# Kernel optimization log

Hardware: AMD Instinct MI355X
Metric: run time of the kernel (lower is better)

Reference implementation:

```python
import jax, jax.numpy as jnp
import numpy as np

# Tree / model dimensions
L = 1024          # number of leaves (batch rows of x)
F = 128           # num_features
H = 128           # num_dense_units
C = 10            # output_dim (num classes)
N = 2 * L - 1     # full binary tree node count
SPLICE = [0, F*H, F*H+H, F*H+H+H*H, F*H+2*H+H*H, F*H+2*H+H*H+H*C, F*H+2*H+H*H+H*C+C]
D = SPLICE[-1]    # 34314 = flattened sub-MLP weight count (layer_shape)
MIN_DIST = 1e-7


def setup_inputs() -> dict:
    key = jax.random.key(0)
    k1, k2, k3 = jax.random.split(key, 3)
    x = jax.random.normal(k1, (L, F), dtype=jnp.float32)
    # per-node AdditionLayer weight vectors (trainable deltas)
    W = jax.random.normal(k2, (N, D), dtype=jnp.float32) * 0.02
    heights = jax.random.uniform(k3, (N,), dtype=jnp.float32)
    p = (np.arange(N) - 1) // 2
    p[0] = 0  # root self-parent; root is excluded from the mut-distance term
    parent = jnp.asarray(p, dtype=jnp.int32)
    leaf_idx = jnp.arange(L - 1, N, dtype=jnp.int32)  # leaves in traversal order
    return {"x": x, "W": W, "heights": heights, "parent": parent, "leaf_idx": leaf_idx}


def reference(x, W, heights, parent, leaf_idx):
    n = W.shape[0]
    depth = int(np.log2(n + 1))
    # Effective weights per node = sum of AdditionLayer deltas along root->node path.
    # Level-by-level parent gather (parents at level d-1 are already accumulated).
    eff = W
    for d in range(1, depth):
        s, e = 2 ** d - 1, 2 ** (d + 1) - 1
        eff = eff.at[s:e].add(eff[parent[s:e]])

    # delta_tensor: root uses squared diff vs zero input (= sum(W_root^2));
    # every other node: curr - input = W_node, so sum|W_node| / mut_distance.
    mut = jnp.maximum(jnp.abs(heights - heights[parent]), MIN_DIST)  # [n]
    l1 = jnp.sum(jnp.abs(W), axis=1)                                 # [n]
    delta = jnp.sum(W[0] ** 2) + jnp.sum(l1[1:] / mut[1:])
    delta = jnp.reshape(delta, (1,))

    # Leaf sub-MLP: splice each leaf's effective weight vector into kernels/biases
    wl = eff[leaf_idx]                                  # [L, D]
    Lf = wl.shape[0]
    W0 = wl[:, SPLICE[0]:SPLICE[1]].reshape(Lf, F, H)
    b0 = wl[:, SPLICE[1]:SPLICE[2]]
    W1 = wl[:, SPLICE[2]:SPLICE[3]].reshape(Lf, H, H)
    b1 = wl[:, SPLICE[3]:SPLICE[4]]
    W2 = wl[:, SPLICE[4]:SPLICE[5]].reshape(Lf, H, C)
    b2 = wl[:, SPLICE[5]:SPLICE[6]]
    h = jax.nn.relu(jnp.einsum('lf,lfh->lh', x, W0) + b0)
    h = jax.nn.relu(jnp.einsum('lh,lhk->lk', h, W1) + b1)
    out = jax.nn.softmax(jnp.einsum('lh,lhc->lc', h, W2) + b2, axis=-1)
    return (out, delta)
```

## Files before the change

kernel.cpp:

```cpp
#include <hip/hip_runtime.h>

#define LN 1024
#define FF 128
#define HH 128
#define CC 10
#define DD 34314
#define OFF_W0 0
#define OFF_B0 16384
#define OFF_W1 16512
#define OFF_B1 32896
#define OFF_W2 33024
#define OFF_B2 34304

__global__ void init_delta(float* delta) { *delta = 0.f; }

__device__ __forceinline__ float invmut(const float* h, int node, int par) {
    return 1.f / fmaxf(fabsf(h[node] - h[par]), 1e-7f);
}

__global__ __launch_bounds__(1024, 4) void fused_kernel(const float* __restrict__ W,
                                                        const float* __restrict__ x,
                                                        const float* __restrict__ heights,
                                                        float* __restrict__ out,
                                                        float* __restrict__ delta_out) {
    const int bid  = blockIdx.x;
    const int m    = ((bid & 7) << 5) | (bid >> 3);
    const int tid  = threadIdx.x;
    const int lane = tid & 63;
    const int wv   = tid >> 6;
    const int j2   = lane;

    int path[9];
    {
        int n = 255 + m;
#pragma unroll
        for (int k = 0; k < 9; ++k) { path[k] = n; n = (n - 1) >> 1; }
    }
    const float* R[15];
#pragma unroll
    for (int k = 0; k < 9; ++k) R[k] = W + (size_t)path[k] * DD;
    const int n9a = 511 + 2 * m, n9b = n9a + 1;
    R[9]  = W + (size_t)n9a * DD;
    R[10] = W + (size_t)n9b * DD;
#pragma unroll
    for (int q = 0; q < 4; ++q) R[11 + q] = W + (size_t)(1023 + 4 * m + q) * DD;

    float wgt[15];
#pragma unroll
    for (int k = 0; k < 8; ++k)
        wgt[k] = ((m & ((1 << k) - 1)) == 0) ? invmut(heights, path[k], path[k + 1]) : 0.f;
    wgt[8]  = 0.f;
    wgt[9]  = invmut(heights, n9a, path[0]);
    wgt[10] = invmut(heights, n9b, path[0]);
#pragma unroll
    for (int q = 0; q < 4; ++q)
        wgt[11 + q] = invmut(heights, 1023 + 4 * m + q, (q < 2) ? n9a : n9b);
    const float sqmask = (m == 0) ? 1.f : 0.f;

    __shared__ float ins[4][HH];
    __shared__ float part[4][16][HH];
    __shared__ float lgts[4][CC];
    __shared__ float red[16];

    if (tid < 512) { const int q = tid >> 7, t = tid & 127; ins[q][t] = x[(4 * m + q) * FF + t]; }
    if (tid < 4 * CC) ((float*)lgts)[tid] = 0.f;

    float dacc = 0.f, sacc = 0.f;
    __syncthreads();

#pragma unroll
    for (int layer = 0; layer < 2; ++layer) {
        const int offW = layer ? OFF_W1 : OFF_W0;
        const int offB = layer ? OFF_B1 : OFF_B0;
        const float2* S2[15];
#pragma unroll
        for (int r = 0; r < 15; ++r) S2[r] = reinterpret_cast<const float2*>(R[r] + offW);

        float yx[4], yy[4];
#pragma unroll
        for (int q = 0; q < 4; ++q) { yx[q] = 0.f; yy[q] = 0.f; }

#pragma unroll 2
        for (int i = 0; i < 8; ++i) {
            const int f   = (wv << 3) + i;
            const int off = (f << 6) + j2;
            float ex = 0.f, ey = 0.f;
#pragma unroll
            for (int k = 0; k < 9; ++k) {
                const float2 w = S2[k][off];
                ex += w.x; ey += w.y;
                dacc += (fabsf(w.x) + fabsf(w.y)) * wgt[k];
                if (k == 8) sacc += w.x * w.x + w.y * w.y;
            }
            const float2 wa0 = S2[9][off];
            const float2 wa1 = S2[10][off];
            dacc += (fabsf(wa0.x) + fabsf(wa0.y)) * wgt[9];
            dacc += (fabsf(wa1.x) + fabsf(wa1.y)) * wgt[10];
#pragma unroll
            for (int q = 0; q < 4; ++q) {
                const float2 wb = S2[11 + q][off];
                dacc += (fabsf(wb.x) + fabsf(wb.y)) * wgt[11 + q];
                const float2 wa = (q < 2) ? wa0 : wa1;
                const float xv = ins[q][f];
                yx[q] += xv * (ex + wa.x + wb.x);
                yy[q] += xv * (ey + wa.y + wb.y);
            }
        }
#pragma unroll
        for (int q = 0; q < 4; ++q)
            *reinterpret_cast<float2*>(&part[q][wv][2 * j2]) = make_float2(yx[q], yy[q]);
        __syncthreads();

        if (tid < 512) {
            const int q = tid >> 7, col = tid & 127;
            float eb = 0.f;
#pragma unroll
            for (int k = 0; k < 9; ++k) {
                const float v = R[k][offB + col];
                eb += v;
                if (q == 0) { dacc += fabsf(v) * wgt[k]; if (k == 8) sacc += v * v; }
            }
            const float a0 = R[9][offB + col];
            const float a1 = R[10][offB + col];
            if (q == 0) dacc += fabsf(a0) * wgt[9];
            if (q == 2) dacc += fabsf(a1) * wgt[10];
            const float bq = R[11 + q][offB + col];
            dacc += fabsf(bq) * wgt[11 + q];
            float s = eb + ((q < 2) ? a0 : a1) + bq;
#pragma unroll
            for (int w = 0; w < 16; ++w) s += part[q][w][col];
            ins[q][col] = fmaxf(s, 0.f);
        }
        __syncthreads();
    }

    {
        const float2* S2[15];
#pragma unroll
        for (int r = 0; r < 15; ++r) S2[r] = reinterpret_cast<const float2*>(R[r] + OFF_W2);
        if (tid < 640) {
            const int h  = tid / 5;
            const int c0 = (tid - 5 * h) * 2;
            float ex = 0.f, ey = 0.f;
#pragma unroll
            for (int k = 0; k < 9; ++k) {
                const float2 w = S2[k][tid];
                ex += w.x; ey += w.y;
                dacc += (fabsf(w.x) + fabsf(w.y)) * wgt[k];
                if (k == 8) sacc += w.x * w.x + w.y * w.y;
            }
            const float2 wa0 = S2[9][tid];
            const float2 wa1 = S2[10][tid];
            dacc += (fabsf(wa0.x) + fabsf(wa0.y)) * wgt[9];
            dacc += (fabsf(wa1.x) + fabsf(wa1.y)) * wgt[10];
#pragma unroll
            for (int q = 0; q < 4; ++q) {
                const float2 wb = S2[11 + q][tid];
                dacc += (fabsf(wb.x) + fabsf(wb.y)) * wgt[11 + q];
                const float2 wa = (q < 2) ? wa0 : wa1;
                const float hv = ins[q][h];
                atomicAdd(&lgts[q][c0],     hv * (ex + wa.x + wb.x));
                atomicAdd(&lgts[q][c0 + 1], hv * (ey + wa.y + wb.y));
            }
        }
        __syncthreads();
        if (tid < CC) {
            float eb = 0.f;
#pragma unroll
            for (int k = 0; k < 9; ++k) {
                const float v = R[k][OFF_B2 + tid];
                eb += v;
                dacc += fabsf(v) * wgt[k];
                if (k == 8) sacc += v * v;
            }
            const float a0 = R[9][OFF_B2 + tid];
            const float a1 = R[10][OFF_B2 + tid];
            dacc += fabsf(a0) * wgt[9] + fabsf(a1) * wgt[10];
#pragma unroll
            for (int q = 0; q < 4; ++q) {
                const float bq = R[11 + q][OFF_B2 + tid];
                dacc += fabsf(bq) * wgt[11 + q];
                lgts[q][tid] += eb + ((q < 2) ? a0 : a1) + bq;
            }
        }
        __syncthreads();
    }

    if (tid < 4) {
        const int q = tid;
        float mx = lgts[q][0];
#pragma unroll
        for (int c = 1; c < CC; ++c) mx = fmaxf(mx, lgts[q][c]);
        float e[CC], s = 0.f;
#pragma unroll
        for (int c = 0; c < CC; ++c) { e[c] = expf(lgts[q][c] - mx); s += e[c]; }
        const float inv = 1.f / s;
#pragma unroll
        for (int c = 0; c < CC; ++c) out[(4 * m + q) * CC + c] = e[c] * inv;
    }

    float v = dacc + sacc * sqmask;
    for (int o = 32; o > 0; o >>= 1) v += __shfl_down(v, o);
    if (lane == 0) red[wv] = v;
    __syncthreads();
    if (tid == 0) {
        float s = 0.f;
#pragma unroll
        for (int w = 0; w < 16; ++w) s += red[w];
        atomicAdd(delta_out, s);
    }
}

extern "C" void kernel_launch(void* const* d_in, const int* in_sizes, int n_in,
                              void* d_out, int out_size, void* d_ws, size_t ws_size,
                              hipStream_t stream) {
    const float* x       = (const float*)d_in[0];
    const float* W       = (const float*)d_in[1];
    const float* heights = (const float*)d_in[2];

    float* out   = (float*)d_out;
    float* delta = (float*)d_out + LN * CC;

    init_delta<<<1, 1, 0, stream>>>(delta);
    fused_kernel<<<256, 1024, 0, stream>>>(W, x, heights, out, delta);
}
```

Baseline: 97.08 us.

## Split fused MLP kernel into three per-layer kernels with more blocks

Splits the single 256-block fused kernel into three kernels, one per layer. The two large layers use 1024 blocks of 512 threads, each handling a quarter of the input rows, and write partial products to workspace; the next kernel sums them and applies bias and ReLU. This is meant to raise parallelism and occupancy across the GPU's compute units for the bandwidth-bound weight reads. The cost is extra launches, workspace round-trips, and redundant setup and bias reads per block.

```diff
diff --git a/kernel.cpp b/kernel.cpp
--- a/kernel.cpp
+++ b/kernel.cpp
@@ -18,25 +18,11 @@
     return 1.f / fmaxf(fabsf(h[node] - h[par]), 1e-7f);
 }
 
-__global__ __launch_bounds__(1024, 4) void fused_kernel(const float* __restrict__ W,
-                                                        const float* __restrict__ x,
-                                                        const float* __restrict__ heights,
-                                                        float* __restrict__ out,
-                                                        float* __restrict__ delta_out) {
-    const int bid  = blockIdx.x;
-    const int m    = ((bid & 7) << 5) | (bid >> 3);
-    const int tid  = threadIdx.x;
-    const int lane = tid & 63;
-    const int wv   = tid >> 6;
-    const int j2   = lane;
-
-    int path[9];
-    {
-        int n = 255 + m;
-#pragma unroll
-        for (int k = 0; k < 9; ++k) { path[k] = n; n = (n - 1) >> 1; }
-    }
-    const float* R[15];
+__device__ __forceinline__ void setup(const float* W, const float* heights, int m,
+                                      int* path, const float** R, float* wgt) {
+    int n = 255 + m;
+#pragma unroll
+    for (int k = 0; k < 9; ++k) { path[k] = n; n = (n - 1) >> 1; }
 #pragma unroll
     for (int k = 0; k < 9; ++k) R[k] = W + (size_t)path[k] * DD;
     const int n9a = 511 + 2 * m, n9b = n9a + 1;
@@ -44,8 +30,6 @@
     R[10] = W + (size_t)n9b * DD;
 #pragma unroll
     for (int q = 0; q < 4; ++q) R[11 + q] = W + (size_t)(1023 + 4 * m + q) * DD;
-
-    float wgt[15];
 #pragma unroll
     for (int k = 0; k < 8; ++k)
         wgt[k] = ((m & ((1 << k) - 1)) == 0) ? invmut(heights, path[k], path[k + 1]) : 0.f;
@@ -55,110 +39,247 @@
 #pragma unroll
     for (int q = 0; q < 4; ++q)
         wgt[11 + q] = invmut(heights, 1023 + 4 * m + q, (q < 2) ? n9a : n9b);
-    const float sqmask = (m == 0) ? 1.f : 0.f;
-
-    __shared__ float ins[4][HH];
-    __shared__ float part[4][16][HH];
+}
+
+__global__ __launch_bounds__(512, 8) void k1_w0(const float* __restrict__ W,
+                                                const float* __restrict__ x,
+                                                const float* __restrict__ heights,
+                                                float* __restrict__ ws_y0,
+                                                float* __restrict__ delta_out) {
+    const int bid = blockIdx.x;
+    const int m   = (bid & 7) * 32 + ((bid >> 3) >> 2);
+    const int qt  = (bid >> 3) & 3;
+    const int tid = threadIdx.x, lane = tid & 63, wv = tid >> 6, j2 = lane;
+
+    int path[9]; const float* R[15]; float wgt[15];
+    setup(W, heights, m, path, R, wgt);
+    const float sq = (m == 0) ? 1.f : 0.f;
+
+    __shared__ float xs[4][32];
+    __shared__ float part[4][8][HH];
+    __shared__ float red[8];
+
+    if (tid < 128) { const int q = tid >> 5, f = tid & 31; xs[q][f] = x[(4 * m + q) * FF + qt * 32 + f]; }
+    float dacc = 0.f, sacc = 0.f;
+    float yx[4] = {0.f, 0.f, 0.f, 0.f}, yy[4] = {0.f, 0.f, 0.f, 0.f};
+    __syncthreads();
+
+    const float2* S2[15];
+#pragma unroll
+    for (int r = 0; r < 15; ++r) S2[r] = reinterpret_cast<const float2*>(R[r] + OFF_W0);
+
+#pragma unroll
+    for (int i = 0; i < 4; ++i) {
+        const int fl  = (wv << 2) + i;
+        const int off = (((qt << 5) + fl) << 6) + j2;
+        float ex = 0.f, ey = 0.f;
+#pragma unroll
+        for (int k = 0; k < 9; ++k) {
+            const float2 w = S2[k][off];
+            ex += w.x; ey += w.y;
+            dacc += (fabsf(w.x) + fabsf(w.y)) * wgt[k];
+            if (k == 8) sacc += w.x * w.x + w.y * w.y;
+        }
+        const float2 wa0 = S2[9][off];
+        const float2 wa1 = S2[10][off];
+        dacc += (fabsf(wa0.x) + fabsf(wa0.y)) * wgt[9];
+        dacc += (fabsf(wa1.x) + fabsf(wa1.y)) * wgt[10];
+#pragma unroll
+        for (int q = 0; q < 4; ++q) {
+            const float2 wb = S2[11 + q][off];
+            dacc += (fabsf(wb.x) + fabsf(wb.y)) * wgt[11 + q];
+            const float2 wa = (q < 2) ? wa0 : wa1;
+            const float xv = xs[q][fl];
+            yx[q] += xv * (ex + wa.x + wb.x);
+            yy[q] += xv * (ey + wa.y + wb.y);
+        }
+    }
+#pragma unroll
+    for (int q = 0; q < 4; ++q)
+        *reinterpret_cast<float2*>(&part[q][wv][2 * j2]) = make_float2(yx[q], yy[q]);
+    __syncthreads();
+    {
+        const int q = tid >> 7, col = tid & 127;
+        float s = 0.f;
+#pragma unroll
+        for (int w = 0; w < 8; ++w) s += part[q][w][col];
+        ws_y0[(((m << 2) + qt) << 9) + tid] = s;
+    }
+    float v = dacc + sacc * sq;
+    for (int o = 32; o > 0; o >>= 1) v += __shfl_down(v, o);
+    if (lane == 0) red[wv] = v;
+    __syncthreads();
+    if (tid == 0) {
+        float s = 0.f;
+#pragma unroll
+        for (int w = 0; w < 8; ++w) s += red[w];
+        atomicAdd(delta_out, s);
+    }
+}
+
+__global__ __launch_bounds__(512, 8) void k2_w1(const float* __restrict__ W,
+                                                const float* __restrict__ heights,
+                                                const float* __restrict__ ws_y0,
+                                                float* __restrict__ ws_y1,
+                                                float* __restrict__ delta_out) {
+    const int bid = blockIdx.x;
+    const int m   = (bid & 7) * 32 + ((bid >> 3) >> 2);
+    const int qt  = (bid >> 3) & 3;
+    const int tid = threadIdx.x, lane = tid & 63, wv = tid >> 6, j2 = lane;
+
+    int path[9]; const float* R[15]; float wgt[15];
+    setup(W, heights, m, path, R, wgt);
+    const float sq = (m == 0) ? 1.f : 0.f;
+
+    __shared__ float hs[4][HH];
+    __shared__ float part[4][8][HH];
+    __shared__ float red[8];
+    float dacc = 0.f, sacc = 0.f;
+
+    {
+        const int q = tid >> 7, col = tid & 127;
+        float s = 0.f;
+#pragma unroll
+        for (int qq = 0; qq < 4; ++qq) s += ws_y0[(((m << 2) + qq) << 9) + tid];
+        float eb = 0.f;
+#pragma unroll
+        for (int k = 0; k < 9; ++k) {
+            const float v = R[k][OFF_B0 + col];
+            eb += v;
+            if (qt == 0 && q == 0) { dacc += fabsf(v) * wgt[k]; if (k == 8) sacc += v * v; }
+        }
+        const float a0 = R[9][OFF_B0 + col];
+        const float a1 = R[10][OFF_B0 + col];
+        if (qt == 0 && q == 0) dacc += fabsf(a0) * wgt[9];
+        if (qt == 0 && q == 2) dacc += fabsf(a1) * wgt[10];
+        const float bq = R[11 + q][OFF_B0 + col];
+        if (qt == 0) dacc += fabsf(bq) * wgt[11 + q];
+        hs[q][col] = fmaxf(s + eb + ((q < 2) ? a0 : a1) + bq, 0.f);
+    }
+    __syncthreads();
+
+    float yx[4] = {0.f, 0.f, 0.f, 0.f}, yy[4] = {0.f, 0.f, 0.f, 0.f};
+    const float2* S2[15];
+#pragma unroll
+    for (int r = 0; r < 15; ++r) S2[r] = reinterpret_cast<const float2*>(R[r] + OFF_W1);
+
+#pragma unroll
+    for (int i = 0; i < 4; ++i) {
+        const int hl  = (wv << 2) + i;
+        const int ha  = (qt << 5) + hl;
+        const int off = (ha << 6) + j2;
+        float ex = 0.f, ey = 0.f;
+#pragma unroll
+        for (int k = 0; k < 9; ++k) {
+            const float2 w = S2[k][off];
+            ex += w.x; ey += w.y;
+            dacc += (fabsf(w.x) + fabsf(w.y)) * wgt[k];
+            if (k == 8) sacc += w.x * w.x + w.y * w.y;
+        }
+        const float2 wa0 = S2[9][off];
+        const float2 wa1 = S2[10][off];
+        dacc += (fabsf(wa0.x) + fabsf(wa0.y)) * wgt[9];
+        dacc += (fabsf(wa1.x) + fabsf(wa1.y)) * wgt[10];
+#pragma unroll
+        for (int q = 0; q < 4; ++q) {
+            const float2 wb = S2[11 + q][off];
+            dacc += (fabsf(wb.x) + fabsf(wb.y)) * wgt[11 + q];
+            const float2 wa = (q < 2) ? wa0 : wa1;
+            const float hv = hs[q][ha];
+            yx[q] += hv * (ex + wa.x + wb.x);
+            yy[q] += hv * (ey + wa.y + wb.y);
+        }
+    }
+#pragma unroll
+    for (int q = 0; q < 4; ++q)
+        *reinterpret_cast<float2*>(&part[q][wv][2 * j2]) = make_float2(yx[q], yy[q]);
+    __syncthreads();
+    {
+        const int q = tid >> 7, col = tid & 127;
+        float s = 0.f;
+#pragma unroll
+        for (int w = 0; w < 8; ++w) s += part[q][w][col];
+        ws_y1[(((m << 2) + qt) << 9) + tid] = s;
+    }
+    float v = dacc + sacc * sq;
+    for (int o = 32; o > 0; o >>= 1) v += __shfl_down(v, o);
+    if (lane == 0) red[wv] = v;
+    __syncthreads();
+    if (tid == 0) {
+        float s = 0.f;
+#pragma unroll
+        for (int w = 0; w < 8; ++w) s += red[w];
+        atomicAdd(delta_out, s);
+    }
+}
+
+__global__ __launch_bounds__(512, 4) void k3_w2(const float* __restrict__ W,
+                                                const float* __restrict__ heights,
+                                                const float* __restrict__ ws_y1,
+                                                float* __restrict__ out,
+                                                float* __restrict__ delta_out) {
+    const int bid = blockIdx.x;
+    const int m   = ((bid & 7) << 5) | (bid >> 3);
+    const int tid = threadIdx.x, lane = tid & 63, wv = tid >> 6;
+
+    int path[9]; const float* R[15]; float wgt[15];
+    setup(W, heights, m, path, R, wgt);
+    const float sq = (m == 0) ? 1.f : 0.f;
+
+    __shared__ float hs[4][HH];
     __shared__ float lgts[4][CC];
-    __shared__ float red[16];
-
-    if (tid < 512) { const int q = tid >> 7, t = tid & 127; ins[q][t] = x[(4 * m + q) * FF + t]; }
+    __shared__ float red[8];
+    float dacc = 0.f, sacc = 0.f;
+
     if (tid < 4 * CC) ((float*)lgts)[tid] = 0.f;
 
-    float dacc = 0.f, sacc = 0.f;
-    __syncthreads();
-
-#pragma unroll
-    for (int layer = 0; layer < 2; ++layer) {
-        const int offW = layer ? OFF_W1 : OFF_W0;
-        const int offB = layer ? OFF_B1 : OFF_B0;
+    {
+        const int q = tid >> 7, col = tid & 127;
+        float s = 0.f;
+#pragma unroll
+        for (int qq = 0; qq < 4; ++qq) s += ws_y1[(((m << 2) + qq) << 9) + tid];
+        float eb = 0.f;
+#pragma unroll
+        for (int k = 0; k < 9; ++k) {
+            const float v = R[k][OFF_B1 + col];
+            eb += v;
+            if (q == 0) { dacc += fabsf(v) * wgt[k]; if (k == 8) sacc += v * v; }
+        }
+        const float a0 = R[9][OFF_B1 + col];
+        const float a1 = R[10][OFF_B1 + col];
+        if (q == 0) dacc += fabsf(a0) * wgt[9];
+        if (q == 2) dacc += fabsf(a1) * wgt[10];
+        const float bq = R[11 + q][OFF_B1 + col];
+        dacc += fabsf(bq) * wgt[11 + q];
+        hs[q][col] = fmaxf(s + eb + ((q < 2) ? a0 : a1) + bq, 0.f);
+    }
+    __syncthreads();
+
+    {
         const float2* S2[15];
 #pragma unroll
-        for (int r = 0; r < 15; ++r) S2[r] = reinterpret_cast<const float2*>(R[r] + offW);
-
-        float yx[4], yy[4];
-#pragma unroll
-        for (int q = 0; q < 4; ++q) { yx[q] = 0.f; yy[q] = 0.f; }
-
-#pragma unroll 2
-        for (int i = 0; i < 8; ++i) {
-            const int f   = (wv << 3) + i;
-            const int off = (f << 6) + j2;
+        for (int r = 0; r < 15; ++r) S2[r] = reinterpret_cast<const float2*>(R[r] + OFF_W2);
+        for (int i = tid; i < 640; i += 512) {
+            const int h  = i / 5;
+            const int c0 = (i - 5 * h) * 2;
             float ex = 0.f, ey = 0.f;
 #pragma unroll
             for (int k = 0; k < 9; ++k) {
-                const float2 w = S2[k][off];
+                const float2 w = S2[k][i];
                 ex += w.x; ey += w.y;
                 dacc += (fabsf(w.x) + fabsf(w.y)) * wgt[k];
                 if (k == 8) sacc += w.x * w.x + w.y * w.y;
             }
-            const float2 wa0 = S2[9][off];
-            const float2 wa1 = S2[10][off];
+            const float2 wa0 = S2[9][i];
+            const float2 wa1 = S2[10][i];
             dacc += (fabsf(wa0.x) + fabsf(wa0.y)) * wgt[9];
             dacc += (fabsf(wa1.x) + fabsf(wa1.y)) * wgt[10];
 #pragma unroll
             for (int q = 0; q < 4; ++q) {
-                const float2 wb = S2[11 + q][off];
+                const float2 wb = S2[11 + q][i];
                 dacc += (fabsf(wb.x) + fabsf(wb.y)) * wgt[11 + q];
                 const float2 wa = (q < 2) ? wa0 : wa1;
-                const float xv = ins[q][f];
-                yx[q] += xv * (ex + wa.x + wb.x);
-                yy[q] += xv * (ey + wa.y + wb.y);
-            }
-        }
-#pragma unroll
-        for (int q = 0; q < 4; ++q)
-            *reinterpret_cast<float2*>(&part[q][wv][2 * j2]) = make_float2(yx[q], yy[q]);
-        __syncthreads();
-
-        if (tid < 512) {
-            const int q = tid >> 7, col = tid & 127;
-            float eb = 0.f;
-#pragma unroll
-            for (int k = 0; k < 9; ++k) {
-                const float v = R[k][offB + col];
-                eb += v;
-                if (q == 0) { dacc += fabsf(v) * wgt[k]; if (k == 8) sacc += v * v; }
-            }
-            const float a0 = R[9][offB + col];
-            const float a1 = R[10][offB + col];
-            if (q == 0) dacc += fabsf(a0) * wgt[9];
-            if (q == 2) dacc += fabsf(a1) * wgt[10];
-            const float bq = R[11 + q][offB + col];
-            dacc += fabsf(bq) * wgt[11 + q];
-            float s = eb + ((q < 2) ? a0 : a1) + bq;
-#pragma unroll
-            for (int w = 0; w < 16; ++w) s += part[q][w][col];
-            ins[q][col] = fmaxf(s, 0.f);
-        }
-        __syncthreads();
-    }
-
-    {
-        const float2* S2[15];
-#pragma unroll
-        for (int r = 0; r < 15; ++r) S2[r] = reinterpret_cast<const float2*>(R[r] + OFF_W2);
-        if (tid < 640) {
-            const int h  = tid / 5;
-            const int c0 = (tid - 5 * h) * 2;
-            float ex = 0.f, ey = 0.f;
-#pragma unroll
-            for (int k = 0; k < 9; ++k) {
-                const float2 w = S2[k][tid];
-                ex += w.x; ey += w.y;
-                dacc += (fabsf(w.x) + fabsf(w.y)) * wgt[k];
-                if (k == 8) sacc += w.x * w.x + w.y * w.y;
-            }
-            const float2 wa0 = S2[9][tid];
-            const float2 wa1 = S2[10][tid];
-            dacc += (fabsf(wa0.x) + fabsf(wa0.y)) * wgt[9];
-            dacc += (fabsf(wa1.x) + fabsf(wa1.y)) * wgt[10];
-#pragma unroll
-            for (int q = 0; q < 4; ++q) {
-                const float2 wb = S2[11 + q][tid];
-                dacc += (fabsf(wb.x) + fabsf(wb.y)) * wgt[11 + q];
-                const float2 wa = (q < 2) ? wa0 : wa1;
-                const float hv = ins[q][h];
+                const float hv = hs[q][h];
                 atomicAdd(&lgts[q][c0],     hv * (ex + wa.x + wb.x));
                 atomicAdd(&lgts[q][c0 + 1], hv * (ey + wa.y + wb.y));
             }
@@ -199,14 +320,14 @@
         for (int c = 0; c < CC; ++c) out[(4 * m + q) * CC + c] = e[c] * inv;
     }
 
-    float v = dacc + sacc * sqmask;
+    float v = dacc + sacc * sq;
     for (int o = 32; o > 0; o >>= 1) v += __shfl_down(v, o);
     if (lane == 0) red[wv] = v;
     __syncthreads();
     if (tid == 0) {
         float s = 0.f;
 #pragma unroll
-        for (int w = 0; w < 16; ++w) s += red[w];
+        for (int w = 0; w < 8; ++w) s += red[w];
         atomicAdd(delta_out, s);
     }
 }
@@ -220,7 +341,11 @@
 
     float* out   = (float*)d_out;
     float* delta = (float*)d_out + LN * CC;
+    float* ws_y0 = (float*)d_ws;
+    float* ws_y1 = (float*)d_ws + 256 * 4 * 512;
 
     init_delta<<<1, 1, 0, stream>>>(delta);
-    fused_kernel<<<256, 1024, 0, stream>>>(W, x, heights, out, delta);
-}
+    k1_w0<<<1024, 512, 0, stream>>>(W, x, heights, ws_y0, delta);
+    k2_w1<<<1024, 512, 0, stream>>>(W, heights, ws_y0, ws_y1, delta);
+    k3_w2<<<256, 512, 0, stream>>>(W, heights, ws_y1, out, delta);
+}
```

Result: slower. 223.7 us (+130.4%).

## Split work into 512 blocks of two leaves with shared ancestor sum staging

Applied to the files above, without the earlier changes.

Each block now handles one level-9 node and its two leaf children instead of four leaves, which doubles the grid to 512 blocks. The summed ancestor weights for each layer are staged in a 32KB shared buffer in two halves and then combined with each leaf's own delta. Per-node weights are made wave-uniform with readfirstlane. This adds parallelism and occupancy, at the cost of re-reading the ancestor path (ten rows per block versus eleven shared by four leaves), which raises total global traffic and adds extra barriers.

```diff
diff --git a/kernel.cpp b/kernel.cpp
--- a/kernel.cpp
+++ b/kernel.cpp
@@ -18,115 +18,120 @@
     return 1.f / fmaxf(fabsf(h[node] - h[par]), 1e-7f);
 }
 
-__global__ __launch_bounds__(1024, 4) void fused_kernel(const float* __restrict__ W,
-                                                        const float* __restrict__ x,
-                                                        const float* __restrict__ heights,
-                                                        float* __restrict__ out,
-                                                        float* __restrict__ delta_out) {
+__device__ __forceinline__ float sgpr(float v) {
+    return __uint_as_float(__builtin_amdgcn_readfirstlane(__float_as_uint(v)));
+}
+
+__global__ __launch_bounds__(1024, 8) void fused2(const float* __restrict__ W,
+                                                  const float* __restrict__ x,
+                                                  const float* __restrict__ heights,
+                                                  float* __restrict__ out,
+                                                  float* __restrict__ delta_out) {
     const int bid  = blockIdx.x;
-    const int m    = ((bid & 7) << 5) | (bid >> 3);
+    const int b    = ((bid & 7) << 6) | (bid >> 3);
     const int tid  = threadIdx.x;
     const int lane = tid & 63;
     const int wv   = tid >> 6;
-    const int j2   = lane;
-
-    int path[9];
-    {
-        int n = 255 + m;
-#pragma unroll
-        for (int k = 0; k < 9; ++k) { path[k] = n; n = (n - 1) >> 1; }
-    }
-    const float* R[15];
-#pragma unroll
-    for (int k = 0; k < 9; ++k) R[k] = W + (size_t)path[k] * DD;
-    const int n9a = 511 + 2 * m, n9b = n9a + 1;
-    R[9]  = W + (size_t)n9a * DD;
-    R[10] = W + (size_t)n9b * DD;
-#pragma unroll
-    for (int q = 0; q < 4; ++q) R[11 + q] = W + (size_t)(1023 + 4 * m + q) * DD;
-
-    float wgt[15];
-#pragma unroll
-    for (int k = 0; k < 8; ++k)
-        wgt[k] = ((m & ((1 << k) - 1)) == 0) ? invmut(heights, path[k], path[k + 1]) : 0.f;
-    wgt[8]  = 0.f;
-    wgt[9]  = invmut(heights, n9a, path[0]);
-    wgt[10] = invmut(heights, n9b, path[0]);
-#pragma unroll
-    for (int q = 0; q < 4; ++q)
-        wgt[11 + q] = invmut(heights, 1023 + 4 * m + q, (q < 2) ? n9a : n9b);
-    const float sqmask = (m == 0) ? 1.f : 0.f;
-
-    __shared__ float ins[4][HH];
-    __shared__ float part[4][16][HH];
-    __shared__ float lgts[4][CC];
+
+    int path[10];
+    path[0] = 511 + b;
+#pragma unroll
+    for (int k = 1; k < 10; ++k) path[k] = (path[k - 1] - 1) >> 1;
+
+    const float* R[12];
+#pragma unroll
+    for (int k = 0; k < 10; ++k) R[k] = W + (size_t)path[k] * DD;
+    const int leafn0 = 1023 + 2 * b;
+    R[10] = W + (size_t)leafn0 * DD;
+    R[11] = W + (size_t)(leafn0 + 1) * DD;
+
+    float wgt[10];
+#pragma unroll
+    for (int k = 0; k < 9; ++k) {
+        const bool own = (b & ((1 << k) - 1)) == 0;
+        wgt[k] = sgpr(own ? invmut(heights, path[k], path[k + 1]) : 0.f);
+    }
+    wgt[9] = 0.f;
+    const float wl0 = sgpr(invmut(heights, leafn0, path[0]));
+    const float wl1 = sgpr(invmut(heights, leafn0 + 1, path[0]));
+    const float sqm = (b == 0) ? 1.f : 0.f;
+
+    __shared__ float esum[8192];
+    __shared__ float part[2][16][128];
+    __shared__ float ins[2][128];
+    __shared__ float ebias[128];
+    __shared__ float lgts[2][CC];
     __shared__ float red[16];
 
-    if (tid < 512) { const int q = tid >> 7, t = tid & 127; ins[q][t] = x[(4 * m + q) * FF + t]; }
-    if (tid < 4 * CC) ((float*)lgts)[tid] = 0.f;
+    if (tid < 256) { const int q = tid >> 7, t = tid & 127; ins[q][t] = x[(2 * b + q) * FF + t]; }
+    if (tid < 2 * CC) ((float*)lgts)[tid] = 0.f;
 
     float dacc = 0.f, sacc = 0.f;
-    __syncthreads();
 
 #pragma unroll
     for (int layer = 0; layer < 2; ++layer) {
         const int offW = layer ? OFF_W1 : OFF_W0;
         const int offB = layer ? OFF_B1 : OFF_B0;
-        const float2* S2[15];
-#pragma unroll
-        for (int r = 0; r < 15; ++r) S2[r] = reinterpret_cast<const float2*>(R[r] + offW);
-
-        float yx[4], yy[4];
-#pragma unroll
-        for (int q = 0; q < 4; ++q) { yx[q] = 0.f; yy[q] = 0.f; }
-
+        const float2* S2[12];
+#pragma unroll
+        for (int r = 0; r < 12; ++r) S2[r] = reinterpret_cast<const float2*>(R[r] + offW);
+
+        float yx0 = 0.f, yy0 = 0.f, yx1 = 0.f, yy1 = 0.f;
+#pragma unroll
+        for (int half = 0; half < 2; ++half) {
+            __syncthreads();
+#pragma unroll 1
+            for (int it = 0; it < 4; ++it) {
+                const int i   = it * 1024 + tid;
+                const int pos = half * 4096 + i;
+                float2 wd[10];
+#pragma unroll
+                for (int k = 0; k < 10; ++k) wd[k] = S2[k][pos];
+                float ex = 0.f, ey = 0.f;
+#pragma unroll
+                for (int k = 0; k < 10; ++k) {
+                    ex += wd[k].x; ey += wd[k].y;
+                    dacc += (fabsf(wd[k].x) + fabsf(wd[k].y)) * wgt[k];
+                }
+                sacc += wd[9].x * wd[9].x + wd[9].y * wd[9].y;
+                *reinterpret_cast<float2*>(&esum[2 * i]) = make_float2(ex, ey);
+            }
+            __syncthreads();
 #pragma unroll 2
-        for (int i = 0; i < 8; ++i) {
-            const int f   = (wv << 3) + i;
-            const int off = (f << 6) + j2;
-            float ex = 0.f, ey = 0.f;
-#pragma unroll
-            for (int k = 0; k < 9; ++k) {
-                const float2 w = S2[k][off];
-                ex += w.x; ey += w.y;
-                dacc += (fabsf(w.x) + fabsf(w.y)) * wgt[k];
-                if (k == 8) sacc += w.x * w.x + w.y * w.y;
-            }
-            const float2 wa0 = S2[9][off];
-            const float2 wa1 = S2[10][off];
-            dacc += (fabsf(wa0.x) + fabsf(wa0.y)) * wgt[9];
-            dacc += (fabsf(wa1.x) + fabsf(wa1.y)) * wgt[10];
-#pragma unroll
-            for (int q = 0; q < 4; ++q) {
-                const float2 wb = S2[11 + q][off];
-                dacc += (fabsf(wb.x) + fabsf(wb.y)) * wgt[11 + q];
-                const float2 wa = (q < 2) ? wa0 : wa1;
-                const float xv = ins[q][f];
-                yx[q] += xv * (ex + wa.x + wb.x);
-                yy[q] += xv * (ey + wa.y + wb.y);
-            }
-        }
-#pragma unroll
-        for (int q = 0; q < 4; ++q)
-            *reinterpret_cast<float2*>(&part[q][wv][2 * j2]) = make_float2(yx[q], yy[q]);
-        __syncthreads();
-
-        if (tid < 512) {
+            for (int it = 0; it < 4; ++it) {
+                const int i   = it * 1024 + tid;
+                const int pos = half * 4096 + i;
+                const int f   = half * 64 + 16 * it + wv;
+                const float2 e  = *reinterpret_cast<const float2*>(&esum[2 * i]);
+                const float2 w0 = S2[10][pos];
+                const float2 w1 = S2[11][pos];
+                dacc += (fabsf(w0.x) + fabsf(w0.y)) * wl0;
+                dacc += (fabsf(w1.x) + fabsf(w1.y)) * wl1;
+                const float xv0 = ins[0][f];
+                const float xv1 = ins[1][f];
+                yx0 += xv0 * (e.x + w0.x); yy0 += xv0 * (e.y + w0.y);
+                yx1 += xv1 * (e.x + w1.x); yy1 += xv1 * (e.y + w1.y);
+            }
+        }
+        *reinterpret_cast<float2*>(&part[0][wv][2 * lane]) = make_float2(yx0, yy0);
+        *reinterpret_cast<float2*>(&part[1][wv][2 * lane]) = make_float2(yx1, yy1);
+        if (tid < 128) {
+            float eb = 0.f;
+#pragma unroll
+            for (int k = 0; k < 10; ++k) {
+                const float v = R[k][offB + tid];
+                eb += v;
+                dacc += fabsf(v) * wgt[k];
+                if (k == 9) sacc += v * v;
+            }
+            ebias[tid] = eb;
+        }
+        __syncthreads();
+        if (tid < 256) {
             const int q = tid >> 7, col = tid & 127;
-            float eb = 0.f;
-#pragma unroll
-            for (int k = 0; k < 9; ++k) {
-                const float v = R[k][offB + col];
-                eb += v;
-                if (q == 0) { dacc += fabsf(v) * wgt[k]; if (k == 8) sacc += v * v; }
-            }
-            const float a0 = R[9][offB + col];
-            const float a1 = R[10][offB + col];
-            if (q == 0) dacc += fabsf(a0) * wgt[9];
-            if (q == 2) dacc += fabsf(a1) * wgt[10];
-            const float bq = R[11 + q][offB + col];
-            dacc += fabsf(bq) * wgt[11 + q];
-            float s = eb + ((q < 2) ? a0 : a1) + bq;
+            const float bq = R[10 + q][offB + col];
+            dacc += fabsf(bq) * (q ? wl1 : wl0);
+            float s = ebias[col] + bq;
 #pragma unroll
             for (int w = 0; w < 16; ++w) s += part[q][w][col];
             ins[q][col] = fmaxf(s, 0.f);
@@ -135,58 +140,53 @@
     }
 
     {
-        const float2* S2[15];
-#pragma unroll
-        for (int r = 0; r < 15; ++r) S2[r] = reinterpret_cast<const float2*>(R[r] + OFF_W2);
+        const float2* S2[12];
+#pragma unroll
+        for (int r = 0; r < 12; ++r) S2[r] = reinterpret_cast<const float2*>(R[r] + OFF_W2);
         if (tid < 640) {
-            const int h  = tid / 5;
-            const int c0 = (tid - 5 * h) * 2;
+            const int pos = tid;
+            float2 wd[10];
+#pragma unroll
+            for (int k = 0; k < 10; ++k) wd[k] = S2[k][pos];
             float ex = 0.f, ey = 0.f;
 #pragma unroll
-            for (int k = 0; k < 9; ++k) {
-                const float2 w = S2[k][tid];
-                ex += w.x; ey += w.y;
-                dacc += (fabsf(w.x) + fabsf(w.y)) * wgt[k];
-                if (k == 8) sacc += w.x * w.x + w.y * w.y;
-            }
-            const float2 wa0 = S2[9][tid];
-            const float2 wa1 = S2[10][tid];
-            dacc += (fabsf(wa0.x) + fabsf(wa0.y)) * wgt[9];
-            dacc += (fabsf(wa1.x) + fabsf(wa1.y)) * wgt[10];
-#pragma unroll
-            for (int q = 0; q < 4; ++q) {
-                const float2 wb = S2[11 + q][tid];
-                dacc += (fabsf(wb.x) + fabsf(wb.y)) * wgt[11 + q];
-                const float2 wa = (q < 2) ? wa0 : wa1;
-                const float hv = ins[q][h];
-                atomicAdd(&lgts[q][c0],     hv * (ex + wa.x + wb.x));
-                atomicAdd(&lgts[q][c0 + 1], hv * (ey + wa.y + wb.y));
-            }
+            for (int k = 0; k < 10; ++k) {
+                ex += wd[k].x; ey += wd[k].y;
+                dacc += (fabsf(wd[k].x) + fabsf(wd[k].y)) * wgt[k];
+            }
+            sacc += wd[9].x * wd[9].x + wd[9].y * wd[9].y;
+            const float2 w0 = S2[10][pos];
+            const float2 w1 = S2[11][pos];
+            dacc += (fabsf(w0.x) + fabsf(w0.y)) * wl0;
+            dacc += (fabsf(w1.x) + fabsf(w1.y)) * wl1;
+            const int h  = pos / 5;
+            const int c0 = 2 * (pos - 5 * h);
+            const float hv0 = ins[0][h], hv1 = ins[1][h];
+            atomicAdd(&lgts[0][c0],     hv0 * (ex + w0.x));
+            atomicAdd(&lgts[0][c0 + 1], hv0 * (ey + w0.y));
+            atomicAdd(&lgts[1][c0],     hv1 * (ex + w1.x));
+            atomicAdd(&lgts[1][c0 + 1], hv1 * (ey + w1.y));
         }
         __syncthreads();
         if (tid < CC) {
             float eb = 0.f;
 #pragma unroll
-            for (int k = 0; k < 9; ++k) {
+            for (int k = 0; k < 10; ++k) {
                 const float v = R[k][OFF_B2 + tid];
                 eb += v;
                 dacc += fabsf(v) * wgt[k];
-                if (k == 8) sacc += v * v;
-            }
-            const float a0 = R[9][OFF_B2 + tid];
-            const float a1 = R[10][OFF_B2 + tid];
-            dacc += fabsf(a0) * wgt[9] + fabsf(a1) * wgt[10];
-#pragma unroll
-            for (int q = 0; q < 4; ++q) {
-                const float bq = R[11 + q][OFF_B2 + tid];
-                dacc += fabsf(bq) * wgt[11 + q];
-                lgts[q][tid] += eb + ((q < 2) ? a0 : a1) + bq;
-            }
-        }
-        __syncthreads();
-    }
-
-    if (tid < 4) {
+                if (k == 9) sacc += v * v;
+            }
+            const float b0q = R[10][OFF_B2 + tid];
+            const float b1q = R[11][OFF_B2 + tid];
+            dacc += fabsf(b0q) * wl0 + fabsf(b1q) * wl1;
+            lgts[0][tid] += eb + b0q;
+            lgts[1][tid] += eb + b1q;
+        }
+        __syncthreads();
+    }
+
+    if (tid < 2) {
         const int q = tid;
         float mx = lgts[q][0];
 #pragma unroll
@@ -196,10 +196,10 @@
         for (int c = 0; c < CC; ++c) { e[c] = expf(lgts[q][c] - mx); s += e[c]; }
         const float inv = 1.f / s;
 #pragma unroll
-        for (int c = 0; c < CC; ++c) out[(4 * m + q) * CC + c] = e[c] * inv;
-    }
-
-    float v = dacc + sacc * sqmask;
+        for (int c = 0; c < CC; ++c) out[(2 * b + q) * CC + c] = e[c] * inv;
+    }
+
+    float v = dacc + sacc * sqm;
     for (int o = 32; o > 0; o >>= 1) v += __shfl_down(v, o);
     if (lane == 0) red[wv] = v;
     __syncthreads();
@@ -222,5 +222,5 @@
     float* delta = (float*)d_out + LN * CC;
 
     init_delta<<<1, 1, 0, stream>>>(delta);
-    fused_kernel<<<256, 1024, 0, stream>>>(W, x, heights, out, delta);
-}
+    fused2<<<512, 1024, 0, stream>>>(W, x, heights, out, delta);
+}
```

Result: slower. 138.0 us (+42.1%).
